# Performance work log

Measured on AMD Instinct MI355X. Metric: run time of the kernel, lower is better.

The kernel has to match this reference:

```python
import jax, jax.numpy as jnp
import numpy as np

N_NODES = 100000
N_EDGES = 1600000
IN_C, HID_C, OUT_C = 128, 128, 40
BN_EPS = 1e-5


def gcn_conv(x, W, b, edge_index, n):
    # PyG GCNConv: h = x @ W, add self-loops, symmetric normalization, scatter-add to targets, + bias
    h = x @ W  # [N, C_out]
    loops = jnp.arange(n, dtype=edge_index.dtype)
    src = jnp.concatenate([edge_index[0], loops])  # messages flow source -> target
    dst = jnp.concatenate([edge_index[1], loops])
    deg = jax.ops.segment_sum(jnp.ones_like(dst, dtype=h.dtype), dst, num_segments=n)
    dinv = jnp.where(deg > 0, jax.lax.rsqrt(deg), 0.0).astype(h.dtype)
    norm = dinv[src] * dinv[dst]  # [E+N]
    msg = h[src] * norm[:, None]
    out = jax.ops.segment_sum(msg, dst, num_segments=n)
    return out + b


def batch_norm(x, gamma, beta):
    # training-mode batchnorm over the node dimension (biased variance, as torch)
    mean = jnp.mean(x, axis=0)
    var = jnp.mean(jnp.square(x - mean), axis=0)
    return (x - mean) * jax.lax.rsqrt(var + BN_EPS) * gamma + beta


def setup_inputs() -> dict:
    key = jax.random.key(0)
    ks = jax.random.split(key, 8)
    x = jax.random.normal(ks[0], (N_NODES, IN_C), dtype=jnp.float32)
    edge_index = jax.random.randint(ks[1], (2, N_EDGES), 0, N_NODES, dtype=jnp.int64)
    def glorot(k, fi, fo):
        s = np.sqrt(6.0 / (fi + fo)).astype(np.float32)
        return jax.random.uniform(k, (fi, fo), jnp.float32, -s, s)
    return {
        "x": x,
        "edge_index": edge_index,
        "W1": glorot(ks[2], IN_C, HID_C), "b1": jnp.zeros((HID_C,), jnp.float32),
        "g1": jnp.ones((HID_C,), jnp.float32), "bt1": jnp.zeros((HID_C,), jnp.float32),
        "W2": glorot(ks[3], HID_C, HID_C), "b2": jnp.zeros((HID_C,), jnp.float32),
        "g2": jnp.ones((HID_C,), jnp.float32), "bt2": jnp.zeros((HID_C,), jnp.float32),
        "W3": glorot(ks[4], HID_C, OUT_C), "b3": jnp.zeros((OUT_C,), jnp.float32),
    }


def reference(x, edge_index, W1, b1, g1, bt1, W2, b2, g2, bt2, W3, b3):
    n = x.shape[0]
    # layer 1: GCNConv -> BatchNorm -> ReLU (dropout p=0.0 / eval -> identity)
    h = gcn_conv(x, W1, b1, edge_index, n)
    h = jax.nn.relu(batch_norm(h, g1, bt1))
    # layer 2
    h = gcn_conv(h, W2, b2, edge_index, n)
    h = jax.nn.relu(batch_norm(h, g2, bt2))
    # output layer (no norm/act)
    return gcn_conv(h, W3, b3, edge_index, n)
```

## Files before the change

kernel.cpp:

```cpp
#include <hip/hip_runtime.h>
#include <hip/hip_fp16.h>
#include <cstdint>

#define BN_EPS 1e-5f
#define PCHUNK 4096
#define BCAP 16384

typedef _Float16 f16;
typedef _Float16 f16x8 __attribute__((ext_vector_type(8)));
typedef _Float16 f16x4 __attribute__((ext_vector_type(4)));
typedef float f32x4 __attribute__((ext_vector_type(4)));


__device__ __forceinline__ void load_edge(const void* eb, int E, bool w64,
                                          int e, int& s, int& d) {
  if (w64) {
    const long long* p = (const long long*)eb;
    s = (int)p[e];
    d = (int)p[E + e];
  } else {
    const int* p = (const int*)eb;
    s = p[e];
    d = p[E + e];
  }
}

__global__ __launch_bounds__(256) void part_k(const void* __restrict__ eb, int E,
                                              int* __restrict__ realtot,
                                              int* __restrict__ pcur,
                                              int2* __restrict__ part) {
  __shared__ int hist[256], lofs[256], gbase[256], lcur[256];
  __shared__ int sa[256], sb[256];
  __shared__ int2 stage[PCHUNK];
  __shared__ int w64f;
  const int t = threadIdx.x;
  const int e0 = blockIdx.x * PCHUNK;
  const int cnt = min(PCHUNK, E - e0);
  hist[t] = 0;
  if (t == 0) w64f = 0;
  __syncthreads();
  {
    const unsigned* w = (const unsigned*)eb;
    int nz = 0;
    int cov = min(cnt, 512);
    for (int k = t; k < cov; k += 256) nz |= (w[2 * (size_t)(e0 + k) + 1] != 0u);
    if (nz) atomicOr(&w64f, 1);
  }
  __syncthreads();
  const bool w64 = (w64f == 0);
  int2 ed[16];
#pragma unroll
  for (int k = 0; k < 16; k++) {
    int idx = t + k * 256;
    if (idx < cnt) {
      int s, d;
      load_edge(eb, E, w64, e0 + idx, s, d);
      ed[k].x = s;
      ed[k].y = d;
      atomicAdd(&hist[d >> 9], 1);
    }
  }
  __syncthreads();
  sa[t] = hist[t];
  __syncthreads();
  int* src = sa;
  int* dst = sb;
  for (int off = 1; off < 256; off <<= 1) {
    int val = src[t] + (t >= off ? src[t - off] : 0);
    dst[t] = val;
    __syncthreads();
    int* tmp = src; src = dst; dst = tmp;
  }
  int c = hist[t];
  lofs[t] = src[t] - c;
  int cpad = (c + 7) & ~7;
  gbase[t] = (c > 0) ? (t * BCAP + atomicAdd(&pcur[t], cpad)) : 0;
  if (c > 0) atomicAdd(&realtot[t], c);
  lcur[t] = src[t] - c;
  __syncthreads();
#pragma unroll
  for (int k = 0; k < 16; k++) {
    int idx = t + k * 256;
    if (idx < cnt) {
      int b = ed[k].y >> 9;
      int p = atomicAdd(&lcur[b], 1);
      stage[p] = ed[k];
    }
  }
  __syncthreads();
  for (int idx = t; idx < cnt; idx += 256) {
    int2 e = stage[idx];
    int b = e.y >> 9;
    part[gbase[b] + (idx - lofs[b])] = e;
  }
  if (c > 0) {
    for (int k = c; k < cpad; k++) part[gbase[t] + k] = make_int2(0, -1);
  }
}

__global__ __launch_bounds__(512) void sort_k(const int2* __restrict__ part,
                                              const int* __restrict__ pcur,
                                              const int* __restrict__ realtot,
                                              int* __restrict__ rp,
                                              float* __restrict__ dinv,
                                              int* __restrict__ csr, int n, int E,
                                              int nbkt) {
  __shared__ int lhist[512], lcur[512];
  __shared__ int sa[512], sb[512];
  const int b = blockIdx.x;
  const int d0 = b << 9;
  const int t = threadIdx.x;
  const int nloc = min(512, n - d0);
  int pacc = 0;
  for (int j = t; j < b; j += 512) pacc += realtot[j];
  sa[t] = pacc;
  __syncthreads();
  for (int off = 256; off > 0; off >>= 1) {
    if (t < off) sa[t] += sa[t + off];
    __syncthreads();
  }
  const int rbase = sa[0];
  __syncthreads();

  lhist[t] = 0;
  __syncthreads();
  const int base = b * BCAP;
  const int T = pcur[b];
  for (int idx = t; idx < T; idx += 512) {
    int2 e = part[base + idx];
    if (e.y >= 0) atomicAdd(&lhist[e.y - d0], 1);
  }
  __syncthreads();
  sa[t] = lhist[t];
  __syncthreads();
  int* src = sa;
  int* dst = sb;
  for (int off = 1; off < 512; off <<= 1) {
    int val = src[t] + (t >= off ? src[t - off] : 0);
    dst[t] = val;
    __syncthreads();
    int* tmp = src; src = dst; dst = tmp;
  }
  int c = lhist[t];
  int gpos = rbase + src[t] - c;
  if (t < nloc) {
    rp[d0 + t] = gpos;
    dinv[d0 + t] = rsqrtf((float)(c + 1));
  }
  lcur[t] = gpos;
  if (b == nbkt - 1 && t == 0) rp[n] = E;
  __syncthreads();
  for (int idx = t; idx < T; idx += 512) {
    int2 e = part[base + idx];
    if (e.y >= 0) {
      int pos = atomicAdd(&lcur[e.y - d0], 1);
      csr[pos] = e.x;
    }
  }
}

__global__ void prep_all(const float* __restrict__ W1, const float* __restrict__ W2,
                         const float* __restrict__ W3, f16* __restrict__ Wt1,
                         f16* __restrict__ Wt2, f16* __restrict__ Wt3) {
  int b = blockIdx.x, k = threadIdx.x;
  if (b < 128) {
    Wt1[(size_t)b * 128 + k] = (f16)W1[(size_t)k * 128 + b];
  } else if (b < 256) {
    int nc = b - 128;
    Wt2[(size_t)nc * 128 + k] = (f16)W2[(size_t)k * 128 + nc];
  } else {
    int nc = b - 256;
    Wt3[(size_t)nc * 128 + k] = (nc < 40) ? (f16)W3[(size_t)k * 40 + nc] : (f16)0.f;
  }
}

template <int NCP, bool BN, bool F32IN>
__global__ __launch_bounds__(256) void gemm_mfma(const void* __restrict__ Xv,
                                                 const f16* __restrict__ Wt,
                                                 const float* __restrict__ bn_acc,
                                                 const float* __restrict__ g,
                                                 const float* __restrict__ bt,
                                                 float inv_n,
                                                 const float* __restrict__ dinv,
                                                 f16* __restrict__ H, int n) {
  constexpr int CB = NCP / 16;
  __shared__ f16 Xs[128][136];
  __shared__ f16 Ws[NCP][136];
  __shared__ float bnS[128], bnH[128];
  const int t = threadIdx.x;
  const int m0 = blockIdx.x * 128;

  if (BN) {
    if (t < 128) {
      float mean = bn_acc[t] * inv_n;
      float var = bn_acc[128 + t] * inv_n - mean * mean;
      float sc = g[t] * rsqrtf(var + BN_EPS);
      bnS[t] = sc;
      bnH[t] = fmaf(-mean, sc, bt[t]);
    }
    __syncthreads();
  }

  if constexpr (F32IN) {
    const float* X = (const float*)Xv;
#pragma unroll
    for (int p = 0; p < 16; p++) {
      int idx = p * 256 + t;
      int row = idx >> 5, c = (idx & 31) * 4;
      float4 v = make_float4(0.f, 0.f, 0.f, 0.f);
      if (m0 + row < n) v = *(const float4*)&X[(size_t)(m0 + row) * 128 + c];
      if (BN) {
        v.x = fmaxf(fmaf(v.x, bnS[c + 0], bnH[c + 0]), 0.f);
        v.y = fmaxf(fmaf(v.y, bnS[c + 1], bnH[c + 1]), 0.f);
        v.z = fmaxf(fmaf(v.z, bnS[c + 2], bnH[c + 2]), 0.f);
        v.w = fmaxf(fmaf(v.w, bnS[c + 3], bnH[c + 3]), 0.f);
      }
      f16x4 h = {(f16)v.x, (f16)v.y, (f16)v.z, (f16)v.w};
      *(f16x4*)&Xs[row][c] = h;
    }
  } else {
    const f16* X = (const f16*)Xv;
#pragma unroll
    for (int p = 0; p < 8; p++) {
      int idx = p * 256 + t;
      int row = idx >> 4, c = (idx & 15) * 8;
      f16x8 v = {0, 0, 0, 0, 0, 0, 0, 0};
      if (m0 + row < n) v = *(const f16x8*)&X[(size_t)(m0 + row) * 128 + c];
      if (BN) {
#pragma unroll
        for (int j = 0; j < 8; j++) {
          float f = (float)v[j];
          f = fmaxf(fmaf(f, bnS[c + j], bnH[c + j]), 0.f);
          v[j] = (f16)f;
        }
      }
      *(f16x8*)&Xs[row][c] = v;
    }
  }
#pragma unroll
  for (int idx = t; idx < NCP * 16; idx += 256) {
    int row = idx >> 4, c = (idx & 15) * 8;
    *(f16x8*)&Ws[row][c] = *(const f16x8*)&Wt[(size_t)row * 128 + c];
  }
  __syncthreads();

  const int w = t >> 6, l = t & 63;
  const int lr = l & 15, lq = l >> 4;
  f32x4 acc[2][CB];
#pragma unroll
  for (int i = 0; i < 2; i++)
#pragma unroll
    for (int j = 0; j < CB; j++) acc[i][j] = (f32x4){0.f, 0.f, 0.f, 0.f};

#pragma unroll
  for (int kb = 0; kb < 4; kb++) {
    f16x8 xf0 = *(const f16x8*)&Xs[w * 32 + lr][kb * 32 + lq * 8];
    f16x8 xf1 = *(const f16x8*)&Xs[w * 32 + 16 + lr][kb * 32 + lq * 8];
#pragma unroll
    for (int cb = 0; cb < CB; cb++) {
      f16x8 wf = *(const f16x8*)&Ws[cb * 16 + lr][kb * 32 + lq * 8];
      acc[0][cb] = __builtin_amdgcn_mfma_f32_16x16x32_f16(wf, xf0, acc[0][cb], 0, 0, 0);
      acc[1][cb] = __builtin_amdgcn_mfma_f32_16x16x32_f16(wf, xf1, acc[1][cb], 0, 0, 0);
    }
  }
#pragma unroll
  for (int rg = 0; rg < 2; rg++) {
    int row = m0 + w * 32 + rg * 16 + lr;
    if (row >= n) continue;
    float dv = dinv[row];
#pragma unroll
    for (int cb = 0; cb < CB; cb++) {
      int col = cb * 16 + lq * 4;
      f32x4 a = acc[rg][cb];
      f16x4 h = {(f16)(a[0] * dv), (f16)(a[1] * dv), (f16)(a[2] * dv),
                 (f16)(a[3] * dv)};
      *(f16x4*)&H[(size_t)row * NCP + col] = h;
    }
  }
}

__global__ __launch_bounds__(256) void agg128h(const f16* __restrict__ H,
                                               const int* __restrict__ rp,
                                               const int* __restrict__ csr,
                                               const float* __restrict__ dinv,
                                               const float* __restrict__ bias,
                                               f16* __restrict__ out, int n) {
  const int lane = threadIdx.x & 63;
  const int sub = lane >> 4;
  const int cl = lane & 15;
  const int gw = (blockIdx.x * 256 + threadIdx.x) >> 6;
  const int nw = (gridDim.x * 256) >> 6;
  const int nquads = (n + 3) >> 2;
  for (int q = gw; q < nquads; q += nw) {
    const int i = q * 4 + sub;
    const bool valid = (i < n);
    const int ic = valid ? i : 0;
    f16x8 hv = *(const f16x8*)&H[(size_t)ic * 128 + cl * 8];
    float a[8];
#pragma unroll
    for (int c = 0; c < 8; c++) a[c] = (float)hv[c];
    int e0 = rp[ic];
    int cnt = valid ? (rp[ic + 1] - e0) : 0;
    int m = max(cnt, __shfl_xor(cnt, 16));
    m = max(m, __shfl_xor(m, 32));
    int j = 0;
    for (; j + 8 <= m; j += 8) {
      int ss[8];
#pragma unroll
      for (int k = 0; k < 8; k++) ss[k] = csr[(j + k < cnt) ? e0 + j + k : 0];
      f16x8 vv[8];
#pragma unroll
      for (int k = 0; k < 8; k++)
        vv[k] = *(const f16x8*)&H[(size_t)ss[k] * 128 + cl * 8];
#pragma unroll
      for (int k = 0; k < 8; k++) {
        float wk = (j + k < cnt) ? 1.f : 0.f;
#pragma unroll
        for (int c = 0; c < 8; c++) a[c] = fmaf((float)vv[k][c], wk, a[c]);
      }
    }
    for (; j < m; j++) {
      int s0 = csr[(j < cnt) ? e0 + j : 0];
      f16x8 v0 = *(const f16x8*)&H[(size_t)s0 * 128 + cl * 8];
      float wk = (j < cnt) ? 1.f : 0.f;
#pragma unroll
      for (int c = 0; c < 8; c++) a[c] = fmaf((float)v0[c], wk, a[c]);
    }
    if (valid) {
      float dv = dinv[ic];
      float4 b0 = *(const float4*)&bias[cl * 8];
      float4 b1 = *(const float4*)&bias[cl * 8 + 4];
      f16x8 h;
      h[0] = (f16)fmaf(a[0], dv, b0.x);
      h[1] = (f16)fmaf(a[1], dv, b0.y);
      h[2] = (f16)fmaf(a[2], dv, b0.z);
      h[3] = (f16)fmaf(a[3], dv, b0.w);
      h[4] = (f16)fmaf(a[4], dv, b1.x);
      h[5] = (f16)fmaf(a[5], dv, b1.y);
      h[6] = (f16)fmaf(a[6], dv, b1.z);
      h[7] = (f16)fmaf(a[7], dv, b1.w);
      *(f16x8*)&out[(size_t)i * 128 + cl * 8] = h;
    }
  }
}

__global__ __launch_bounds__(256) void agg64h(const f16* __restrict__ H,
                                              const int* __restrict__ rp,
                                              const int* __restrict__ csr,
                                              const float* __restrict__ dinv,
                                              const float* __restrict__ bias,
                                              float* __restrict__ out, int n) {
  const int lane = threadIdx.x & 63;
  const int sub = lane >> 4;
  const int cl = lane & 15;
  const int gw = (blockIdx.x * 256 + threadIdx.x) >> 6;
  const int nw = (gridDim.x * 256) >> 6;
  const int nquads = (n + 3) >> 2;
  for (int q = gw; q < nquads; q += nw) {
    const int i = q * 4 + sub;
    const bool valid = (i < n);
    const int ic = valid ? i : 0;
    f16x4 hv = *(const f16x4*)&H[(size_t)ic * 64 + cl * 4];
    float a0 = (float)hv[0], a1 = (float)hv[1], a2 = (float)hv[2],
          a3 = (float)hv[3];
    int e0 = rp[ic];
    int cnt = valid ? (rp[ic + 1] - e0) : 0;
    int m = max(cnt, __shfl_xor(cnt, 16));
    m = max(m, __shfl_xor(m, 32));
    int j = 0;
    for (; j + 8 <= m; j += 8) {
      int ss[8];
#pragma unroll
      for (int k = 0; k < 8; k++) ss[k] = csr[(j + k < cnt) ? e0 + j + k : 0];
      f16x4 vv[8];
#pragma unroll
      for (int k = 0; k < 8; k++)
        vv[k] = *(const f16x4*)&H[(size_t)ss[k] * 64 + cl * 4];
#pragma unroll
      for (int k = 0; k < 8; k++) {
        float wk = (j + k < cnt) ? 1.f : 0.f;
        a0 = fmaf((float)vv[k][0], wk, a0);
        a1 = fmaf((float)vv[k][1], wk, a1);
        a2 = fmaf((float)vv[k][2], wk, a2);
        a3 = fmaf((float)vv[k][3], wk, a3);
      }
    }
    for (; j < m; j++) {
      int s0 = csr[(j < cnt) ? e0 + j : 0];
      f16x4 v0 = *(const f16x4*)&H[(size_t)s0 * 64 + cl * 4];
      float wk = (j < cnt) ? 1.f : 0.f;
      a0 = fmaf((float)v0[0], wk, a0);
      a1 = fmaf((float)v0[1], wk, a1);
      a2 = fmaf((float)v0[2], wk, a2);
      a3 = fmaf((float)v0[3], wk, a3);
    }
    if (valid && cl < 10) {
      float dv = dinv[ic];
      float4 bb = *(const float4*)&bias[cl * 4];
      float4 o;
      o.x = fmaf(a0, dv, bb.x);
      o.y = fmaf(a1, dv, bb.y);
      o.z = fmaf(a2, dv, bb.z);
      o.w = fmaf(a3, dv, bb.w);
      *(float4*)&out[(size_t)i * 40 + cl * 4] = o;
    }
  }
}

__global__ __launch_bounds__(256) void bn_stats_h(const f16* __restrict__ H, int n,
                                                  float* __restrict__ acc) {
  int t = threadIdx.x;
  int c2 = t & 63;
  int rg = t >> 6;
  float2 s = {0.f, 0.f}, s2 = {0.f, 0.f};
  for (int r = blockIdx.x * 4 + rg; r < n; r += gridDim.x * 4) {
    float2 v = __half22float2(*(const __half2*)&H[(size_t)r * 128 + c2 * 2]);
    s.x += v.x;
    s.y += v.y;
    s2.x = fmaf(v.x, v.x, s2.x);
    s2.y = fmaf(v.y, v.y, s2.y);
  }
  __shared__ float ls[4][128], ls2[4][128];
  ls[rg][c2 * 2] = s.x;
  ls[rg][c2 * 2 + 1] = s.y;
  ls2[rg][c2 * 2] = s2.x;
  ls2[rg][c2 * 2 + 1] = s2.y;
  __syncthreads();
  if (t < 128) {
    float a_ = ls[0][t] + ls[1][t] + ls[2][t] + ls[3][t];
    float b_ = ls2[0][t] + ls2[1][t] + ls2[2][t] + ls2[3][t];
    atomicAdd(&acc[t], a_);
    atomicAdd(&acc[128 + t], b_);
  }
}

extern "C" void kernel_launch(void* const* d_in, const int* in_sizes, int n_in,
                              void* d_out, int out_size, void* d_ws, size_t ws_size,
                              hipStream_t stream) {
  const float* x = (const float*)d_in[0];
  const void* eb = d_in[1];
  const float* W1 = (const float*)d_in[2];
  const float* b1 = (const float*)d_in[3];
  const float* g1 = (const float*)d_in[4];
  const float* bt1 = (const float*)d_in[5];
  const float* W2 = (const float*)d_in[6];
  const float* b2 = (const float*)d_in[7];
  const float* g2 = (const float*)d_in[8];
  const float* bt2 = (const float*)d_in[9];
  const float* W3 = (const float*)d_in[10];
  const float* b3 = (const float*)d_in[11];

  const int n = in_sizes[0] / 128;
  const int E = in_sizes[1] / 2;
  const float inv_n = 1.0f / (float)n;

  char* w = (char*)d_ws;
  auto alloc = [&](size_t bytes) {
    void* p = (void*)w;
    w += (bytes + 255) & ~(size_t)255;
    return p;
  };
  const int NBKT = (n + 511) / 512;
  f16* hA = (f16*)alloc((size_t)n * 128 * 2);
  f16* hB = (f16*)alloc((size_t)n * 128 * 2);
  int* csr = (int*)alloc((size_t)E * 4);
  int2* part = (int2*)alloc((size_t)NBKT * BCAP * 8);
  float* dinv = (float*)alloc((size_t)n * 4);
  int* rp = (int*)alloc((size_t)(n + 1) * 4);
  f16* Wt1 = (f16*)alloc(128 * 128 * 2);
  f16* Wt2 = (f16*)alloc(128 * 128 * 2);
  f16* Wt3 = (f16*)alloc(64 * 128 * 2);
  int* pcur = (int*)alloc(256 * 4);
  int* realtot = (int*)alloc(256 * 4);
  float* bn_acc1 = (float*)alloc(256 * 4);
  float* bn_acc2 = (float*)alloc(256 * 4);
  size_t zbytes = (char*)bn_acc2 + 256 * 4 - (char*)pcur;
  hipMemsetAsync(pcur, 0, zbytes, stream);

  const int PB = (E + PCHUNK - 1) / PCHUNK;

  prep_all<<<320, 128, 0, stream>>>(W1, W2, W3, Wt1, Wt2, Wt3);

  part_k<<<PB, 256, 0, stream>>>(eb, E, realtot, pcur, part);
  sort_k<<<NBKT, 512, 0, stream>>>(part, pcur, realtot, rp, dinv, csr, n, E, NBKT);

  const int GB = (n + 127) / 128;
  const int AGB = 4096;

  gemm_mfma<128, false, true><<<GB, 256, 0, stream>>>(x, Wt1, nullptr, nullptr,
                                                      nullptr, inv_n, dinv, hA, n);
  agg128h<<<AGB, 256, 0, stream>>>(hA, rp, csr, dinv, b1, hB, n);
  bn_stats_h<<<1024, 256, 0, stream>>>(hB, n, bn_acc1);
  gemm_mfma<128, true, false><<<GB, 256, 0, stream>>>(hB, Wt2, bn_acc1, g1, bt1,
                                                      inv_n, dinv, hA, n);
  agg128h<<<AGB, 256, 0, stream>>>(hA, rp, csr, dinv, b2, hB, n);
  bn_stats_h<<<1024, 256, 0, stream>>>(hB, n, bn_acc2);
  gemm_mfma<64, true, false><<<GB, 256, 0, stream>>>(hB, Wt3, bn_acc2, g2, bt2,
                                                     inv_n, dinv, hA, n);
  agg64h<<<AGB, 256, 0, stream>>>(hA, rp, csr, dinv, b3, (float*)d_out, n);
}
```

Measured before the change: 436.1 us.

## Pad CSR rows to multiples of eight with sentinel zero row, simplify aggregation

Each destination bucket's CSR is now laid out at a fixed per-bucket capacity, with every row padded to a multiple of 8 using a sentinel index n. The GEMM writes a zero row at index n so padded gathers add nothing. This removes the global prefix sum over bucket totals and the per-edge masking in aggregation. The aggregation kernels become one quad per wave with vectorized int4 index loads and fp16 vector adds instead of fp32 FMA accumulation, which risks precision loss. part_k moves to 512 threads per block.

Result: faster. 422.2 us (-3.2%).

```diff
diff --git a/kernel.cpp b/kernel.cpp
--- a/kernel.cpp
+++ b/kernel.cpp
@@ -5,6 +5,7 @@
 #define BN_EPS 1e-5f
 #define PCHUNK 4096
 #define BCAP 16384
+#define CSRCAP 16384
 
 typedef _Float16 f16;
 typedef _Float16 f16x8 __attribute__((ext_vector_type(8)));
@@ -25,8 +26,7 @@
   }
 }
 
-__global__ __launch_bounds__(256) void part_k(const void* __restrict__ eb, int E,
-                                              int* __restrict__ realtot,
+__global__ __launch_bounds__(512) void part_k(const void* __restrict__ eb, int E,
                                               int* __restrict__ pcur,
                                               int2* __restrict__ part) {
   __shared__ int hist[256], lofs[256], gbase[256], lcur[256];
@@ -36,22 +36,22 @@
   const int t = threadIdx.x;
   const int e0 = blockIdx.x * PCHUNK;
   const int cnt = min(PCHUNK, E - e0);
-  hist[t] = 0;
+  if (t < 256) hist[t] = 0;
   if (t == 0) w64f = 0;
   __syncthreads();
   {
     const unsigned* w = (const unsigned*)eb;
     int nz = 0;
     int cov = min(cnt, 512);
-    for (int k = t; k < cov; k += 256) nz |= (w[2 * (size_t)(e0 + k) + 1] != 0u);
+    for (int k = t; k < cov; k += 512) nz |= (w[2 * (size_t)(e0 + k) + 1] != 0u);
     if (nz) atomicOr(&w64f, 1);
   }
   __syncthreads();
   const bool w64 = (w64f == 0);
-  int2 ed[16];
-#pragma unroll
-  for (int k = 0; k < 16; k++) {
-    int idx = t + k * 256;
+  int2 ed[8];
+#pragma unroll
+  for (int k = 0; k < 8; k++) {
+    int idx = t + k * 512;
     if (idx < cnt) {
       int s, d;
       load_edge(eb, E, w64, e0 + idx, s, d);
@@ -61,26 +61,30 @@
     }
   }
   __syncthreads();
-  sa[t] = hist[t];
+  if (t < 256) sa[t] = hist[t];
   __syncthreads();
   int* src = sa;
   int* dst = sb;
   for (int off = 1; off < 256; off <<= 1) {
-    int val = src[t] + (t >= off ? src[t - off] : 0);
-    dst[t] = val;
+    int val = 0;
+    if (t < 256) val = src[t] + (t >= off ? src[t - off] : 0);
+    __syncthreads();
+    if (t < 256) dst[t] = val;
     __syncthreads();
     int* tmp = src; src = dst; dst = tmp;
   }
-  int c = hist[t];
-  lofs[t] = src[t] - c;
-  int cpad = (c + 7) & ~7;
-  gbase[t] = (c > 0) ? (t * BCAP + atomicAdd(&pcur[t], cpad)) : 0;
-  if (c > 0) atomicAdd(&realtot[t], c);
-  lcur[t] = src[t] - c;
-  __syncthreads();
-#pragma unroll
-  for (int k = 0; k < 16; k++) {
-    int idx = t + k * 256;
+  int c = 0;
+  if (t < 256) {
+    c = hist[t];
+    lofs[t] = src[t] - c;
+    int cpad = (c + 7) & ~7;
+    gbase[t] = (c > 0) ? (t * BCAP + atomicAdd(&pcur[t], cpad)) : 0;
+    lcur[t] = src[t] - c;
+  }
+  __syncthreads();
+#pragma unroll
+  for (int k = 0; k < 8; k++) {
+    int idx = t + k * 512;
     if (idx < cnt) {
       int b = ed[k].y >> 9;
       int p = atomicAdd(&lcur[b], 1);
@@ -88,40 +92,28 @@
     }
   }
   __syncthreads();
-  for (int idx = t; idx < cnt; idx += 256) {
+  for (int idx = t; idx < cnt; idx += 512) {
     int2 e = stage[idx];
     int b = e.y >> 9;
     part[gbase[b] + (idx - lofs[b])] = e;
   }
-  if (c > 0) {
+  if (t < 256 && c > 0) {
+    int cpad = (c + 7) & ~7;
     for (int k = c; k < cpad; k++) part[gbase[t] + k] = make_int2(0, -1);
   }
 }
 
 __global__ __launch_bounds__(512) void sort_k(const int2* __restrict__ part,
                                               const int* __restrict__ pcur,
-                                              const int* __restrict__ realtot,
-                                              int* __restrict__ rp,
+                                              int2* __restrict__ rpc,
                                               float* __restrict__ dinv,
-                                              int* __restrict__ csr, int n, int E,
-                                              int nbkt) {
-  __shared__ int lhist[512], lcur[512];
+                                              int* __restrict__ csr, int n) {
+  __shared__ int lhist[512], lcur[512], lstart[512];
   __shared__ int sa[512], sb[512];
   const int b = blockIdx.x;
   const int d0 = b << 9;
   const int t = threadIdx.x;
   const int nloc = min(512, n - d0);
-  int pacc = 0;
-  for (int j = t; j < b; j += 512) pacc += realtot[j];
-  sa[t] = pacc;
-  __syncthreads();
-  for (int off = 256; off > 0; off >>= 1) {
-    if (t < off) sa[t] += sa[t + off];
-    __syncthreads();
-  }
-  const int rbase = sa[0];
-  __syncthreads();
-
   lhist[t] = 0;
   __syncthreads();
   const int base = b * BCAP;
@@ -131,24 +123,26 @@
     if (e.y >= 0) atomicAdd(&lhist[e.y - d0], 1);
   }
   __syncthreads();
-  sa[t] = lhist[t];
+  int c = lhist[t];
+  int cpad = (c + 7) & ~7;
+  sa[t] = cpad;
   __syncthreads();
   int* src = sa;
   int* dst = sb;
   for (int off = 1; off < 512; off <<= 1) {
     int val = src[t] + (t >= off ? src[t - off] : 0);
+    __syncthreads();
     dst[t] = val;
     __syncthreads();
     int* tmp = src; src = dst; dst = tmp;
   }
-  int c = lhist[t];
-  int gpos = rbase + src[t] - c;
+  int start = b * CSRCAP + src[t] - cpad;
   if (t < nloc) {
-    rp[d0 + t] = gpos;
+    rpc[d0 + t] = make_int2(start, cpad);
     dinv[d0 + t] = rsqrtf((float)(c + 1));
   }
-  lcur[t] = gpos;
-  if (b == nbkt - 1 && t == 0) rp[n] = E;
+  lstart[t] = start;
+  lcur[t] = start;
   __syncthreads();
   for (int idx = t; idx < T; idx += 512) {
     int2 e = part[base + idx];
@@ -156,6 +150,9 @@
       int pos = atomicAdd(&lcur[e.y - d0], 1);
       csr[pos] = e.x;
     }
+  }
+  if (t < nloc) {
+    for (int k = c; k < cpad; k++) csr[lstart[t] + k] = n;
   }
 }
 
@@ -266,8 +263,8 @@
 #pragma unroll
   for (int rg = 0; rg < 2; rg++) {
     int row = m0 + w * 32 + rg * 16 + lr;
-    if (row >= n) continue;
-    float dv = dinv[row];
+    if (row > n) continue;
+    float dv = (row < n) ? dinv[row] : 0.f;
 #pragma unroll
     for (int cb = 0; cb < CB; cb++) {
       int col = cb * 16 + lq * 4;
@@ -280,130 +277,95 @@
 }
 
 __global__ __launch_bounds__(256) void agg128h(const f16* __restrict__ H,
-                                               const int* __restrict__ rp,
+                                               const int2* __restrict__ rpc,
                                                const int* __restrict__ csr,
                                                const float* __restrict__ dinv,
                                                const float* __restrict__ bias,
                                                f16* __restrict__ out, int n) {
   const int lane = threadIdx.x & 63;
-  const int sub = lane >> 4;
-  const int cl = lane & 15;
-  const int gw = (blockIdx.x * 256 + threadIdx.x) >> 6;
-  const int nw = (gridDim.x * 256) >> 6;
-  const int nquads = (n + 3) >> 2;
-  for (int q = gw; q < nquads; q += nw) {
-    const int i = q * 4 + sub;
-    const bool valid = (i < n);
-    const int ic = valid ? i : 0;
-    f16x8 hv = *(const f16x8*)&H[(size_t)ic * 128 + cl * 8];
-    float a[8];
-#pragma unroll
-    for (int c = 0; c < 8; c++) a[c] = (float)hv[c];
-    int e0 = rp[ic];
-    int cnt = valid ? (rp[ic + 1] - e0) : 0;
-    int m = max(cnt, __shfl_xor(cnt, 16));
-    m = max(m, __shfl_xor(m, 32));
-    int j = 0;
-    for (; j + 8 <= m; j += 8) {
-      int ss[8];
-#pragma unroll
-      for (int k = 0; k < 8; k++) ss[k] = csr[(j + k < cnt) ? e0 + j + k : 0];
-      f16x8 vv[8];
-#pragma unroll
-      for (int k = 0; k < 8; k++)
-        vv[k] = *(const f16x8*)&H[(size_t)ss[k] * 128 + cl * 8];
-#pragma unroll
-      for (int k = 0; k < 8; k++) {
-        float wk = (j + k < cnt) ? 1.f : 0.f;
-#pragma unroll
-        for (int c = 0; c < 8; c++) a[c] = fmaf((float)vv[k][c], wk, a[c]);
-      }
-    }
-    for (; j < m; j++) {
-      int s0 = csr[(j < cnt) ? e0 + j : 0];
-      f16x8 v0 = *(const f16x8*)&H[(size_t)s0 * 128 + cl * 8];
-      float wk = (j < cnt) ? 1.f : 0.f;
-#pragma unroll
-      for (int c = 0; c < 8; c++) a[c] = fmaf((float)v0[c], wk, a[c]);
-    }
-    if (valid) {
-      float dv = dinv[ic];
-      float4 b0 = *(const float4*)&bias[cl * 8];
-      float4 b1 = *(const float4*)&bias[cl * 8 + 4];
-      f16x8 h;
-      h[0] = (f16)fmaf(a[0], dv, b0.x);
-      h[1] = (f16)fmaf(a[1], dv, b0.y);
-      h[2] = (f16)fmaf(a[2], dv, b0.z);
-      h[3] = (f16)fmaf(a[3], dv, b0.w);
-      h[4] = (f16)fmaf(a[4], dv, b1.x);
-      h[5] = (f16)fmaf(a[5], dv, b1.y);
-      h[6] = (f16)fmaf(a[6], dv, b1.z);
-      h[7] = (f16)fmaf(a[7], dv, b1.w);
-      *(f16x8*)&out[(size_t)i * 128 + cl * 8] = h;
-    }
+  const int sub = lane >> 4, cl = lane & 15;
+  const int q = (blockIdx.x * 256 + threadIdx.x) >> 6;
+  const int i = q * 4 + sub;
+  const bool valid = (i < n);
+  const int ic = valid ? i : 0;
+  f16x8 a = *(const f16x8*)&H[(size_t)ic * 128 + cl * 8];
+  int2 rc = rpc[ic];
+  const int e0 = rc.x, cntp = rc.y;
+  for (int j = 0; j < cntp; j += 8) {
+    int4 c0 = *(const int4*)&csr[e0 + j];
+    int4 c1 = *(const int4*)&csr[e0 + j + 4];
+    f16x8 v0 = *(const f16x8*)&H[(size_t)c0.x * 128 + cl * 8];
+    f16x8 v1 = *(const f16x8*)&H[(size_t)c0.y * 128 + cl * 8];
+    f16x8 v2 = *(const f16x8*)&H[(size_t)c0.z * 128 + cl * 8];
+    f16x8 v3 = *(const f16x8*)&H[(size_t)c0.w * 128 + cl * 8];
+    f16x8 v4 = *(const f16x8*)&H[(size_t)c1.x * 128 + cl * 8];
+    f16x8 v5 = *(const f16x8*)&H[(size_t)c1.y * 128 + cl * 8];
+    f16x8 v6 = *(const f16x8*)&H[(size_t)c1.z * 128 + cl * 8];
+    f16x8 v7 = *(const f16x8*)&H[(size_t)c1.w * 128 + cl * 8];
+    f16x8 t01 = v0 + v1;
+    f16x8 t23 = v2 + v3;
+    f16x8 t45 = v4 + v5;
+    f16x8 t67 = v6 + v7;
+    a = a + ((t01 + t23) + (t45 + t67));
+  }
+  if (valid) {
+    float dv = dinv[ic];
+    float4 b0 = *(const float4*)&bias[cl * 8];
+    float4 b1 = *(const float4*)&bias[cl * 8 + 4];
+    f16x8 h;
+    h[0] = (f16)fmaf((float)a[0], dv, b0.x);
+    h[1] = (f16)fmaf((float)a[1], dv, b0.y);
+    h[2] = (f16)fmaf((float)a[2], dv, b0.z);
+    h[3] = (f16)fmaf((float)a[3], dv, b0.w);
+    h[4] = (f16)fmaf((float)a[4], dv, b1.x);
+    h[5] = (f16)fmaf((float)a[5], dv, b1.y);
+    h[6] = (f16)fmaf((float)a[6], dv, b1.z);
+    h[7] = (f16)fmaf((float)a[7], dv, b1.w);
+    *(f16x8*)&out[(size_t)i * 128 + cl * 8] = h;
   }
 }
 
 __global__ __launch_bounds__(256) void agg64h(const f16* __restrict__ H,
-                                              const int* __restrict__ rp,
+                                              const int2* __restrict__ rpc,
                                               const int* __restrict__ csr,
                                               const float* __restrict__ dinv,
                                               const float* __restrict__ bias,
                                               float* __restrict__ out, int n) {
   const int lane = threadIdx.x & 63;
-  const int sub = lane >> 4;
-  const int cl = lane & 15;
-  const int gw = (blockIdx.x * 256 + threadIdx.x) >> 6;
-  const int nw = (gridDim.x * 256) >> 6;
-  const int nquads = (n + 3) >> 2;
-  for (int q = gw; q < nquads; q += nw) {
-    const int i = q * 4 + sub;
-    const bool valid = (i < n);
-    const int ic = valid ? i : 0;
-    f16x4 hv = *(const f16x4*)&H[(size_t)ic * 64 + cl * 4];
-    float a0 = (float)hv[0], a1 = (float)hv[1], a2 = (float)hv[2],
-          a3 = (float)hv[3];
-    int e0 = rp[ic];
-    int cnt = valid ? (rp[ic + 1] - e0) : 0;
-    int m = max(cnt, __shfl_xor(cnt, 16));
-    m = max(m, __shfl_xor(m, 32));
-    int j = 0;
-    for (; j + 8 <= m; j += 8) {
-      int ss[8];
-#pragma unroll
-      for (int k = 0; k < 8; k++) ss[k] = csr[(j + k < cnt) ? e0 + j + k : 0];
-      f16x4 vv[8];
-#pragma unroll
-      for (int k = 0; k < 8; k++)
-        vv[k] = *(const f16x4*)&H[(size_t)ss[k] * 64 + cl * 4];
-#pragma unroll
-      for (int k = 0; k < 8; k++) {
-        float wk = (j + k < cnt) ? 1.f : 0.f;
-        a0 = fmaf((float)vv[k][0], wk, a0);
-        a1 = fmaf((float)vv[k][1], wk, a1);
-        a2 = fmaf((float)vv[k][2], wk, a2);
-        a3 = fmaf((float)vv[k][3], wk, a3);
-      }
-    }
-    for (; j < m; j++) {
-      int s0 = csr[(j < cnt) ? e0 + j : 0];
-      f16x4 v0 = *(const f16x4*)&H[(size_t)s0 * 64 + cl * 4];
-      float wk = (j < cnt) ? 1.f : 0.f;
-      a0 = fmaf((float)v0[0], wk, a0);
-      a1 = fmaf((float)v0[1], wk, a1);
-      a2 = fmaf((float)v0[2], wk, a2);
-      a3 = fmaf((float)v0[3], wk, a3);
-    }
-    if (valid && cl < 10) {
-      float dv = dinv[ic];
-      float4 bb = *(const float4*)&bias[cl * 4];
-      float4 o;
-      o.x = fmaf(a0, dv, bb.x);
-      o.y = fmaf(a1, dv, bb.y);
-      o.z = fmaf(a2, dv, bb.z);
-      o.w = fmaf(a3, dv, bb.w);
-      *(float4*)&out[(size_t)i * 40 + cl * 4] = o;
-    }
+  const int sub = lane >> 4, cl = lane & 15;
+  const int q = (blockIdx.x * 256 + threadIdx.x) >> 6;
+  const int i = q * 4 + sub;
+  const bool valid = (i < n);
+  const int ic = valid ? i : 0;
+  f16x4 a = *(const f16x4*)&H[(size_t)ic * 64 + cl * 4];
+  int2 rc = rpc[ic];
+  const int e0 = rc.x, cntp = rc.y;
+  for (int j = 0; j < cntp; j += 8) {
+    int4 c0 = *(const int4*)&csr[e0 + j];
+    int4 c1 = *(const int4*)&csr[e0 + j + 4];
+    f16x4 v0 = *(const f16x4*)&H[(size_t)c0.x * 64 + cl * 4];
+    f16x4 v1 = *(const f16x4*)&H[(size_t)c0.y * 64 + cl * 4];
+    f16x4 v2 = *(const f16x4*)&H[(size_t)c0.z * 64 + cl * 4];
+    f16x4 v3 = *(const f16x4*)&H[(size_t)c0.w * 64 + cl * 4];
+    f16x4 v4 = *(const f16x4*)&H[(size_t)c1.x * 64 + cl * 4];
+    f16x4 v5 = *(const f16x4*)&H[(size_t)c1.y * 64 + cl * 4];
+    f16x4 v6 = *(const f16x4*)&H[(size_t)c1.z * 64 + cl * 4];
+    f16x4 v7 = *(const f16x4*)&H[(size_t)c1.w * 64 + cl * 4];
+    f16x4 t01 = v0 + v1;
+    f16x4 t23 = v2 + v3;
+    f16x4 t45 = v4 + v5;
+    f16x4 t67 = v6 + v7;
+    a = a + ((t01 + t23) + (t45 + t67));
+  }
+  if (valid && cl < 10) {
+    float dv = dinv[ic];
+    float4 bb = *(const float4*)&bias[cl * 4];
+    float4 o;
+    o.x = fmaf((float)a[0], dv, bb.x);
+    o.y = fmaf((float)a[1], dv, bb.y);
+    o.z = fmaf((float)a[2], dv, bb.z);
+    o.w = fmaf((float)a[3], dv, bb.w);
+    *(float4*)&out[(size_t)i * 40 + cl * 4] = o;
   }
 }
 
@@ -461,17 +423,16 @@
     return p;
   };
   const int NBKT = (n + 511) / 512;
-  f16* hA = (f16*)alloc((size_t)n * 128 * 2);
-  f16* hB = (f16*)alloc((size_t)n * 128 * 2);
-  int* csr = (int*)alloc((size_t)E * 4);
+  f16* hA = (f16*)alloc((size_t)(n + 1) * 128 * 2);
+  f16* hB = (f16*)alloc((size_t)(n + 1) * 128 * 2);
+  int* csr = (int*)alloc((size_t)NBKT * CSRCAP * 4);
   int2* part = (int2*)alloc((size_t)NBKT * BCAP * 8);
   float* dinv = (float*)alloc((size_t)n * 4);
-  int* rp = (int*)alloc((size_t)(n + 1) * 4);
+  int2* rpc = (int2*)alloc((size_t)n * 8);
   f16* Wt1 = (f16*)alloc(128 * 128 * 2);
   f16* Wt2 = (f16*)alloc(128 * 128 * 2);
   f16* Wt3 = (f16*)alloc(64 * 128 * 2);
   int* pcur = (int*)alloc(256 * 4);
-  int* realtot = (int*)alloc(256 * 4);
   float* bn_acc1 = (float*)alloc(256 * 4);
   float* bn_acc2 = (float*)alloc(256 * 4);
   size_t zbytes = (char*)bn_acc2 + 256 * 4 - (char*)pcur;
@@ -481,21 +442,22 @@
 
   prep_all<<<320, 128, 0, stream>>>(W1, W2, W3, Wt1, Wt2, Wt3);
 
-  part_k<<<PB, 256, 0, stream>>>(eb, E, realtot, pcur, part);
-  sort_k<<<NBKT, 512, 0, stream>>>(part, pcur, realtot, rp, dinv, csr, n, E, NBKT);
-
-  const int GB = (n + 127) / 128;
-  const int AGB = 4096;
+  part_k<<<PB, 512, 0, stream>>>(eb, E, pcur, part);
+  sort_k<<<NBKT, 512, 0, stream>>>(part, pcur, rpc, dinv, csr, n);
+
+  const int GB = (n + 128) / 128;
+  const int NQ = (n + 3) / 4;
+  const int AGB = (NQ + 3) / 4;
 
   gemm_mfma<128, false, true><<<GB, 256, 0, stream>>>(x, Wt1, nullptr, nullptr,
                                                       nullptr, inv_n, dinv, hA, n);
-  agg128h<<<AGB, 256, 0, stream>>>(hA, rp, csr, dinv, b1, hB, n);
+  agg128h<<<AGB, 256, 0, stream>>>(hA, rpc, csr, dinv, b1, hB, n);
   bn_stats_h<<<1024, 256, 0, stream>>>(hB, n, bn_acc1);
   gemm_mfma<128, true, false><<<GB, 256, 0, stream>>>(hB, Wt2, bn_acc1, g1, bt1,
                                                       inv_n, dinv, hA, n);
-  agg128h<<<AGB, 256, 0, stream>>>(hA, rp, csr, dinv, b2, hB, n);
+  agg128h<<<AGB, 256, 0, stream>>>(hA, rpc, csr, dinv, b2, hB, n);
   bn_stats_h<<<1024, 256, 0, stream>>>(hB, n, bn_acc2);
   gemm_mfma<64, true, false><<<GB, 256, 0, stream>>>(hB, Wt3, bn_acc2, g2, bt2,
                                                      inv_n, dinv, hA, n);
-  agg64h<<<AGB, 256, 0, stream>>>(hA, rp, csr, dinv, b3, (float*)d_out, n);
-}
+  agg64h<<<AGB, 256, 0, stream>>>(hA, rpc, csr, dinv, b3, (float*)d_out, n);
+}
```
